# Kernel tuning notes

Measured on AMD Instinct MI355X. Metric: run time of the kernel, lower is better.

## Reference

```python
import jax, jax.numpy as jnp
import numpy as np

EPS = 1e-6
EPS_SQR = EPS ** 2
RADIO = 0.7  # init kwarg
W_STAGE0 = 0.5


def _ohem_mean(diff_flat, k):
    """diff_flat: [B, N] nonneg values; k: [B] int32 per-sample top-k count.
    Equivalent to: mean_i( sum(topk(diff_flat[i], k[i])) / (k[i] + EPS) ).
    Implemented jit-compatibly via descending sort + cumsum + gather."""
    N = diff_flat.shape[-1]
    sorted_desc = -jnp.sort(-diff_flat, axis=-1)          # [B, N]
    csum = jnp.cumsum(sorted_desc, axis=-1)               # [B, N]
    idx = jnp.clip(k - 1, 0, N - 1)
    sum_k = jnp.take_along_axis(csum, idx[:, None], axis=-1)[:, 0]
    sum_k = jnp.where(k > 0, sum_k, jnp.zeros_like(sum_k))
    loss = sum_k / (k.astype(diff_flat.dtype) + EPS)
    return jnp.mean(loss)


def setup_inputs() -> dict:
    key = jax.random.key(0)
    ks = jax.random.split(key, 6)
    B, H, W = 8, 512, 512
    image = jax.random.uniform(ks[0], (B, 3, H, W), dtype=jnp.float32)
    alpha = jax.random.uniform(ks[1], (B, 1, H, W), dtype=jnp.float32) * 255.0  # 0..255 like GT alpha
    raw_alpha_pred = jax.random.uniform(ks[2], (B, 1, H, W), dtype=jnp.float32)
    fg = jax.random.uniform(ks[3], (B, 3, H, W), dtype=jnp.float32)
    bg = jax.random.uniform(ks[4], (B, 3, H, W), dtype=jnp.float32)
    trimap = jax.random.randint(ks[5], (B, 1, H, W), 0, 2, dtype=jnp.int32) * 128  # {0,128}
    return {"image": image, "alpha": alpha, "raw_alpha_pred": raw_alpha_pred,
            "trimap": trimap, "fg": fg, "bg": bg}


def reference(image, alpha, raw_alpha_pred, trimap, fg, bg):
    B = trimap.shape[0]
    unknown = (trimap == 128).astype(image.dtype)          # [B,1,H,W]
    count = jnp.sum(unknown.reshape(B, -1), axis=-1)       # per-sample unknown pixel count
    k = jnp.floor(count * RADIO).astype(jnp.int32)         # torch: int(pred_num * radio)

    # ---- alpha prediction loss ----
    d = (alpha / 255.0 - raw_alpha_pred) * unknown         # [B,1,H,W]
    d = jnp.sqrt(d * d + EPS_SQR)
    alpha_loss = _ohem_mean(d.reshape(B, -1), k)

    # ---- compositional loss ----
    pred_img = fg * raw_alpha_pred + (1.0 - raw_alpha_pred) * bg   # [B,3,H,W]
    dc = (image - pred_img) * unknown                      # mask broadcasts over 3 channels
    dc = jnp.sqrt(dc * dc + EPS_SQR)
    dc = dc.sum(axis=1)                                    # [B,H,W]
    comp_loss = _ohem_mean(dc.reshape(B, -1), k)

    return W_STAGE0 * alpha_loss + (1.0 - W_STAGE0) * comp_loss
```

## Files before the change

kernel.cpp:

```cpp
#include <hip/hip_runtime.h>
#include <math.h>

#define NB 8
#define NPIX 262144
#define TPB 256
#define BPS 128
#define PPB (NPIX / BPS)
#define NBF 768
#define ELO 3488
#define BPTF 3
#define EPS2 1e-12f

#define F4E(v,j) (((const float*)&(v))[j])
#define I4E(v,j) (((const int*)&(v))[j])

__device__ __forceinline__ void pixel_vals(float a, float p,
                                           float i0, float i1, float i2,
                                           float f0, float f1, float f2,
                                           float g0, float g1, float g2,
                                           float& d, float& dc)
{
    float diff = a * (1.0f / 255.0f) - p;
    d = sqrtf(diff * diff + EPS2);
    float om = 1.0f - p;
    float e0 = i0 - (f0 * p + om * g0);
    float e1 = i1 - (f1 * p + om * g1);
    float e2 = i2 - (f2 * p + om * g2);
    dc = sqrtf(e0 * e0 + EPS2) + sqrtf(e1 * e1 + EPS2) + sqrtf(e2 * e2 + EPS2);
}

__device__ __forceinline__ int fbin(float v)
{
    int e = (int)(__float_as_uint(v) >> 18) - ELO;
    return e < 0 ? 0 : e;
}

__global__ __launch_bounds__(TPB) void k_hist(
    const float* __restrict__ image, const float* __restrict__ alpha,
    const float* __restrict__ pred, const int* __restrict__ trimap,
    const float* __restrict__ fg, const float* __restrict__ bg,
    unsigned* __restrict__ h1c, float* __restrict__ h1s)
{
    __shared__ unsigned hcnt[2 * NBF];
    __shared__ float    hsum[2 * NBF];
    const int tid = threadIdx.x;
    for (int i = tid; i < 2 * NBF; i += TPB) { hcnt[i] = 0u; hsum[i] = 0.f; }
    __syncthreads();

    const int s = blockIdx.x / BPS;
    const int chunk = blockIdx.x % BPS;
    const int pbase = s * NPIX + chunk * PPB;
    const int cbase = s * 3 * NPIX + chunk * PPB;

    for (int it = 0; it < PPB / (TPB * 4); ++it) {
        const int off = (it * TPB + tid) * 4;
        int4   tm = *(const int4*)(trimap + pbase + off);
        float4 al = *(const float4*)(alpha + pbase + off);
        float4 pr = *(const float4*)(pred + pbase + off);
        float4 i0 = *(const float4*)(image + cbase + off);
        float4 i1 = *(const float4*)(image + cbase + NPIX + off);
        float4 i2 = *(const float4*)(image + cbase + 2 * NPIX + off);
        float4 f0 = *(const float4*)(fg + cbase + off);
        float4 f1 = *(const float4*)(fg + cbase + NPIX + off);
        float4 f2 = *(const float4*)(fg + cbase + 2 * NPIX + off);
        float4 g0 = *(const float4*)(bg + cbase + off);
        float4 g1 = *(const float4*)(bg + cbase + NPIX + off);
        float4 g2 = *(const float4*)(bg + cbase + 2 * NPIX + off);
#pragma unroll
        for (int j = 0; j < 4; ++j) {
            if (I4E(tm, j) == 128) {
                float d, c;
                pixel_vals(F4E(al, j), F4E(pr, j),
                           F4E(i0, j), F4E(i1, j), F4E(i2, j),
                           F4E(f0, j), F4E(f1, j), F4E(f2, j),
                           F4E(g0, j), F4E(g1, j), F4E(g2, j), d, c);
                int bd = fbin(d), bc = fbin(c);
                atomicAdd(&hcnt[bd], 1u);       atomicAdd(&hsum[bd], d);
                atomicAdd(&hcnt[NBF + bc], 1u); atomicAdd(&hsum[NBF + bc], c);
            }
        }
    }
    __syncthreads();

    for (int i = tid; i < 2 * NBF; i += TPB) {
        unsigned cc = hcnt[i];
        if (cc) {
            int arr = (i >= NBF) ? 1 : 0;
            int b = i - arr * NBF;
            atomicAdd(&h1c[(s * 2 + arr) * NBF + b], cc);
            atomicAdd(&h1s[(s * 2 + arr) * NBF + b], hsum[i]);
        }
    }
}

__global__ __launch_bounds__(TPB) void k_final(
    const unsigned* __restrict__ h1c, const float* __restrict__ h1s,
    float* __restrict__ out)
{
    __shared__ unsigned sufB[TPB];
    __shared__ float    sufF[TPB];
    __shared__ unsigned kbc[1];
    const int t = threadIdx.x;
    const int unit = blockIdx.x;

    unsigned cnt[BPTF]; float sm[BPTF];
    unsigned pc = 0; float ps = 0.f;
#pragma unroll
    for (int j = 0; j < BPTF; ++j) {
        cnt[j] = h1c[unit * NBF + t * BPTF + j];
        sm[j]  = h1s[unit * NBF + t * BPTF + j];
        pc += cnt[j]; ps += sm[j];
    }
    sufB[t] = pc; sufF[t] = ps;
    __syncthreads();
    for (int off = 1; off < TPB; off <<= 1) {
        unsigned ac = (t + off < TPB) ? sufB[t + off] : 0u;
        float    as = (t + off < TPB) ? sufF[t + off] : 0.f;
        __syncthreads();
        sufB[t] += ac; sufF[t] += as;
        __syncthreads();
    }
    if (t == 0) kbc[0] = sufB[0];
    __syncthreads();
    unsigned K = kbc[0];
    unsigned kk = (unsigned)(int)floorf((float)K * 0.7f);
    if (kk == 0) return;

    unsigned suf = sufB[t];
    unsigned above = suf - pc;
    if (above < kk && kk <= suf) {
        unsigned c = above;
        float sa = sufF[t] - ps;
        int done = 0;
#pragma unroll
        for (int j = BPTF - 1; j >= 0; --j) {
            if (!done) {
                if (c + cnt[j] >= kk) {
                    unsigned rem = kk - c;
                    float avg = sm[j] / (float)cnt[j];
                    float sum_k = sa + (float)rem * avg;
                    float loss = sum_k / ((float)kk + 1e-6f);
                    atomicAdd(out, 0.0625f * loss);
                    done = 1;
                } else {
                    c += cnt[j]; sa += sm[j];
                }
            }
        }
    }
}

extern "C" void kernel_launch(void* const* d_in, const int* in_sizes, int n_in,
                              void* d_out, int out_size, void* d_ws, size_t ws_size,
                              hipStream_t stream)
{
    const float* image  = (const float*)d_in[0];
    const float* alpha  = (const float*)d_in[1];
    const float* pred   = (const float*)d_in[2];
    const int*   trimap = (const int*)d_in[3];
    const float* fg     = (const float*)d_in[4];
    const float* bg     = (const float*)d_in[5];
    float* out = (float*)d_out;

    char* ws = (char*)d_ws;
    unsigned* h1c = (unsigned*)(ws);
    float*    h1s = (float*)(ws + 16 * NBF * 4);
    const size_t zbytes = 2 * 16 * NBF * 4;

    hipMemsetAsync(d_ws, 0, zbytes, stream);
    hipMemsetAsync(d_out, 0, sizeof(float), stream);
    k_hist<<<NB * BPS, TPB, 0, stream>>>(image, alpha, pred, trimap, fg, bg, h1c, h1s);
    k_final<<<NB * 2, TPB, 0, stream>>>(h1c, h1s, out);
}
```

Before: 131.3 us.

## Privatize histograms per half-block and partition global atomics, single-block final

Each block now keeps two shared-memory histogram copies, one per half of its threads, which spreads out LDS atomic contention. Global histogram flushes are split across 8 partitions by block index, which cuts contention on the global atomics. The final kernel becomes a single block that sums the partitions and writes the output directly, so the separate output memset is no longer needed. The trade-offs are a serial loop over 16 units in one block and a larger workspace to zero.

New measurement: 158.9 us. 21.0% more time.

```diff
diff --git a/kernel.cpp b/kernel.cpp
--- a/kernel.cpp
+++ b/kernel.cpp
@@ -9,6 +9,7 @@
 #define NBF 768
 #define ELO 3488
 #define BPTF 3
+#define NPART 8
 #define EPS2 1e-12f
 
 #define F4E(v,j) (((const float*)&(v))[j])
@@ -41,10 +42,14 @@
     const float* __restrict__ fg, const float* __restrict__ bg,
     unsigned* __restrict__ h1c, float* __restrict__ h1s)
 {
-    __shared__ unsigned hcnt[2 * NBF];
-    __shared__ float    hsum[2 * NBF];
+    __shared__ unsigned hcnt[2][2 * NBF];
+    __shared__ float    hsum[2][2 * NBF];
     const int tid = threadIdx.x;
-    for (int i = tid; i < 2 * NBF; i += TPB) { hcnt[i] = 0u; hsum[i] = 0.f; }
+    const int cp = tid >> 7;
+    for (int i = tid; i < 2 * NBF; i += TPB) {
+        hcnt[0][i] = 0u; hcnt[1][i] = 0u;
+        hsum[0][i] = 0.f; hsum[1][i] = 0.f;
+    }
     __syncthreads();
 
     const int s = blockIdx.x / BPS;
@@ -75,20 +80,22 @@
                            F4E(f0, j), F4E(f1, j), F4E(f2, j),
                            F4E(g0, j), F4E(g1, j), F4E(g2, j), d, c);
                 int bd = fbin(d), bc = fbin(c);
-                atomicAdd(&hcnt[bd], 1u);       atomicAdd(&hsum[bd], d);
-                atomicAdd(&hcnt[NBF + bc], 1u); atomicAdd(&hsum[NBF + bc], c);
+                atomicAdd(&hcnt[cp][bd], 1u);       atomicAdd(&hsum[cp][bd], d);
+                atomicAdd(&hcnt[cp][NBF + bc], 1u); atomicAdd(&hsum[cp][NBF + bc], c);
             }
         }
     }
     __syncthreads();
 
+    const int part = blockIdx.x & (NPART - 1);
     for (int i = tid; i < 2 * NBF; i += TPB) {
-        unsigned cc = hcnt[i];
+        unsigned cc = hcnt[0][i] + hcnt[1][i];
         if (cc) {
             int arr = (i >= NBF) ? 1 : 0;
             int b = i - arr * NBF;
-            atomicAdd(&h1c[(s * 2 + arr) * NBF + b], cc);
-            atomicAdd(&h1s[(s * 2 + arr) * NBF + b], hsum[i]);
+            size_t idx = (size_t)((s * 2 + arr) * NPART + part) * NBF + b;
+            atomicAdd(&h1c[idx], cc);
+            atomicAdd(&h1s[idx], hsum[0][i] + hsum[1][i]);
         }
     }
 }
@@ -99,55 +106,61 @@
 {
     __shared__ unsigned sufB[TPB];
     __shared__ float    sufF[TPB];
-    __shared__ unsigned kbc[1];
+    __shared__ float    accL;
     const int t = threadIdx.x;
-    const int unit = blockIdx.x;
+    if (t == 0) accL = 0.f;
+    __syncthreads();
 
-    unsigned cnt[BPTF]; float sm[BPTF];
-    unsigned pc = 0; float ps = 0.f;
+    for (int unit = 0; unit < 2 * NB; ++unit) {
+        unsigned cnt[BPTF]; float sm[BPTF];
+        unsigned pc = 0; float ps = 0.f;
 #pragma unroll
-    for (int j = 0; j < BPTF; ++j) {
-        cnt[j] = h1c[unit * NBF + t * BPTF + j];
-        sm[j]  = h1s[unit * NBF + t * BPTF + j];
-        pc += cnt[j]; ps += sm[j];
-    }
-    sufB[t] = pc; sufF[t] = ps;
-    __syncthreads();
-    for (int off = 1; off < TPB; off <<= 1) {
-        unsigned ac = (t + off < TPB) ? sufB[t + off] : 0u;
-        float    as = (t + off < TPB) ? sufF[t + off] : 0.f;
+        for (int j = 0; j < BPTF; ++j) {
+            unsigned c = 0; float sv = 0.f;
+            for (int p = 0; p < NPART; ++p) {
+                size_t idx = (size_t)(unit * NPART + p) * NBF + t * BPTF + j;
+                c += h1c[idx]; sv += h1s[idx];
+            }
+            cnt[j] = c; sm[j] = sv;
+            pc += c; ps += sv;
+        }
+        sufB[t] = pc; sufF[t] = ps;
         __syncthreads();
-        sufB[t] += ac; sufF[t] += as;
-        __syncthreads();
-    }
-    if (t == 0) kbc[0] = sufB[0];
-    __syncthreads();
-    unsigned K = kbc[0];
-    unsigned kk = (unsigned)(int)floorf((float)K * 0.7f);
-    if (kk == 0) return;
-
-    unsigned suf = sufB[t];
-    unsigned above = suf - pc;
-    if (above < kk && kk <= suf) {
-        unsigned c = above;
-        float sa = sufF[t] - ps;
-        int done = 0;
+        for (int off = 1; off < TPB; off <<= 1) {
+            unsigned ac = (t + off < TPB) ? sufB[t + off] : 0u;
+            float    as = (t + off < TPB) ? sufF[t + off] : 0.f;
+            __syncthreads();
+            sufB[t] += ac; sufF[t] += as;
+            __syncthreads();
+        }
+        unsigned K = sufB[0];
+        unsigned kk = (unsigned)(int)floorf((float)K * 0.7f);
+        if (kk > 0) {
+            unsigned suf = sufB[t];
+            unsigned above = suf - pc;
+            if (above < kk && kk <= suf) {
+                unsigned c = above;
+                float sa = sufF[t] - ps;
+                int fin = 0;
 #pragma unroll
-        for (int j = BPTF - 1; j >= 0; --j) {
-            if (!done) {
-                if (c + cnt[j] >= kk) {
-                    unsigned rem = kk - c;
-                    float avg = sm[j] / (float)cnt[j];
-                    float sum_k = sa + (float)rem * avg;
-                    float loss = sum_k / ((float)kk + 1e-6f);
-                    atomicAdd(out, 0.0625f * loss);
-                    done = 1;
-                } else {
-                    c += cnt[j]; sa += sm[j];
+                for (int j = BPTF - 1; j >= 0; --j) {
+                    if (!fin) {
+                        if (c + cnt[j] >= kk) {
+                            unsigned rem = kk - c;
+                            float avg = sm[j] / (float)cnt[j];
+                            float sum_k = sa + (float)rem * avg;
+                            atomicAdd(&accL, 0.0625f * (sum_k / ((float)kk + 1e-6f)));
+                            fin = 1;
+                        } else {
+                            c += cnt[j]; sa += sm[j];
+                        }
+                    }
                 }
             }
         }
+        __syncthreads();
     }
+    if (t == 0) out[0] = accL;
 }
 
 extern "C" void kernel_launch(void* const* d_in, const int* in_sizes, int n_in,
@@ -164,11 +177,10 @@
 
     char* ws = (char*)d_ws;
     unsigned* h1c = (unsigned*)(ws);
-    float*    h1s = (float*)(ws + 16 * NBF * 4);
-    const size_t zbytes = 2 * 16 * NBF * 4;
+    float*    h1s = (float*)(ws + 16 * NPART * NBF * 4);
+    const size_t zbytes = 2 * 16 * NPART * NBF * 4;
 
     hipMemsetAsync(d_ws, 0, zbytes, stream);
-    hipMemsetAsync(d_out, 0, sizeof(float), stream);
     k_hist<<<NB * BPS, TPB, 0, stream>>>(image, alpha, pred, trimap, fg, bg, h1c, h1s);
-    k_final<<<NB * 2, TPB, 0, stream>>>(h1c, h1s, out);
+    k_final<<<1, TPB, 0, stream>>>(h1c, h1s, out);
 }
```
